# Performance work log

Hardware: AMD Instinct MI355X
Metric: run time of the kernel (lower is better)

## Reference

```python
import jax, jax.numpy as jnp
import numpy as np

N_A, N_P, N_T = 40000, 100000, 20000
D = 128
OUT = 64
E_AP, E_PT = 500000, 800000


def setup_inputs() -> dict:
    key = jax.random.key(0)
    ks = jax.random.split(key, 24)
    s = 1.0 / np.sqrt(D)
    inp = {
        'x_author': jax.random.normal(ks[0], (N_A, D), jnp.float32),
        'x_paper': jax.random.normal(ks[1], (N_P, D), jnp.float32),
        'x_term': jax.random.normal(ks[2], (N_T, D), jnp.float32),
        'W_l': jax.random.normal(ks[3], (3, 2, 4, D, D), jnp.float32) * s,
        'b_l': jax.random.normal(ks[4], (3, 2, 4, D), jnp.float32) * 0.01,
        'W_r': jax.random.normal(ks[5], (3, 2, 4, D, D), jnp.float32) * s,
        'lin_model_W': jax.random.normal(ks[6], (D, OUT), jnp.float32) * s,
        'lin_model_b': jax.random.normal(ks[7], (OUT,), jnp.float32) * 0.01,
        'lin_temp_W': jax.random.normal(ks[8], (D, OUT), jnp.float32) * s,
        'lin_temp_b': jax.random.normal(ks[9], (OUT,), jnp.float32) * 0.01,
        'lin2_W': jax.random.normal(ks[10], (OUT, 1), jnp.float32) * (1.0 / np.sqrt(OUT)),
        'lin2_b': jnp.ones((1,), jnp.float32),
        'src_ap': jax.random.randint(ks[11], (E_AP,), 0, N_A, jnp.int32),
        'dst_ap': jax.random.randint(ks[12], (E_AP,), 0, N_P, jnp.int32),
        'src_pa': jax.random.randint(ks[13], (E_AP,), 0, N_P, jnp.int32),
        'dst_pa': jax.random.randint(ks[14], (E_AP,), 0, N_A, jnp.int32),
        'src_pt': jax.random.randint(ks[15], (E_PT,), 0, N_P, jnp.int32),
        'dst_pt': jax.random.randint(ks[16], (E_PT,), 0, N_T, jnp.int32),
        'src_tp': jax.random.randint(ks[17], (E_PT,), 0, N_T, jnp.int32),
        'dst_tp': jax.random.randint(ks[18], (E_PT,), 0, N_P, jnp.int32),
    }
    return inp


def _sage(x_src, x_dst, src, dst, n_dst, Wl, bl, Wr):
    # PyG SAGEConv: lin_l(mean_aggr(x_j)) + lin_r(x_dst); lin_r has no bias.
    xj = x_src[src]                                         # [E, D] gather
    ssum = jax.ops.segment_sum(xj, dst, num_segments=n_dst)  # [n_dst, D]
    cnt = jax.ops.segment_sum(jnp.ones((src.shape[0],), x_src.dtype), dst,
                              num_segments=n_dst)
    mean = ssum / jnp.maximum(cnt, 1.0)[:, None]
    return mean @ Wl + bl + x_dst @ Wr


def _hetero_stack(xa, xp, xt, Wl, bl, Wr, edges, relu=True):
    # Wl/bl/Wr: [num_layers, 4, ...]; relation order: a->p, p->a, p->t, t->p.
    (sap, dap, spa, dpa, spt, dpt, stp, dtp) = edges
    n_layers = Wl.shape[0]
    for l in range(n_layers):
        p_new = (_sage(xa, xp, sap, dap, N_P, Wl[l, 0], bl[l, 0], Wr[l, 0])
                 + _sage(xt, xp, stp, dtp, N_P, Wl[l, 3], bl[l, 3], Wr[l, 3]))
        a_new = _sage(xp, xa, spa, dpa, N_A, Wl[l, 1], bl[l, 1], Wr[l, 1])
        t_new = _sage(xp, xt, spt, dpt, N_T, Wl[l, 2], bl[l, 2], Wr[l, 2])
        xa, xp, xt = jax.nn.relu(a_new), jax.nn.relu(p_new), jax.nn.relu(t_new)
    return xa, xp, xt


def reference(x_author, x_paper, x_term, W_l, b_l, W_r,
              lin_model_W, lin_model_b, lin_temp_W, lin_temp_b,
              lin2_W, lin2_b,
              src_ap, dst_ap, src_pa, dst_pa, src_pt, dst_pt, src_tp, dst_tp):
    edges = (src_ap, dst_ap, src_pa, dst_pa, src_pt, dst_pt, src_tp, dst_tp)
    # stack 0: self.model (DBLP) on raw features
    ma, mp, mt = _hetero_stack(x_author, x_paper, x_term,
                               W_l[0], b_l[0], W_r[0], edges)
    logits = ma @ lin_model_W + lin_model_b                  # [N_A, OUT]
    # stack 1: graph_temperature_scale (DBLP) on model's hidden x_dict
    ta, tp_, tt = _hetero_stack(ma, mp, mt, W_l[1], b_l[1], W_r[1], edges)
    ll1 = ta @ lin_temp_W + lin_temp_b                       # [N_A, OUT]
    temperature = ll1 @ lin2_W + lin2_b                      # [N_A, 1]
    # stack 2: self.convs on raw features (dropout = identity in eval mode)
    oa, op, ot = _hetero_stack(x_author, x_paper, x_term,
                               W_l[2], b_l[2], W_r[2], edges)
    return logits / temperature, oa, op, ot
```

## Files before the change

### kernel.cpp

```cpp
#include <hip/hip_runtime.h>
#include <cstdint>

#define N_A 40000
#define N_P 100000
#define N_T 20000
#define D 128
#define OUT_DIM 64
#define E_AP 500000
#define E_PT 800000

typedef __attribute__((ext_vector_type(8))) short bf16x8;
typedef __attribute__((ext_vector_type(4))) float f32x4;

static inline int ceil_div(int a, int b){ return (a + b - 1) / b; }

__device__ inline unsigned short f2bf(float f){
  uint32_t u = __builtin_bit_cast(uint32_t, f);
  uint32_t r = (u + 0x7FFFu + ((u >> 16) & 1u)) >> 16;
  return (unsigned short)r;
}
__device__ inline float bf2f(unsigned short h){
  uint32_t u = ((uint32_t)h) << 16;
  return __builtin_bit_cast(float, u);
}

__global__ void hist_kernel(const int* __restrict__ dst, int E, int* __restrict__ cnt){
  int i = blockIdx.x * blockDim.x + threadIdx.x;
  if (i < E) atomicAdd(&cnt[dst[i]], 1);
}

__global__ void block_sums_kernel(const int* __restrict__ cnt, int n, int* __restrict__ bsums){
  __shared__ int red[256];
  int b = blockIdx.x, t = threadIdx.x;
  int base = b * 1024;
  int s = 0;
  for (int i = t; i < 1024; i += 256){ int idx = base + i; if (idx < n) s += cnt[idx]; }
  red[t] = s; __syncthreads();
  for (int off = 128; off > 0; off >>= 1){ if (t < off) red[t] += red[t + off]; __syncthreads(); }
  if (t == 0) bsums[b] = red[0];
}

__global__ void scan_bsums_kernel(int* bsums, int nb){
  __shared__ int sh[128];
  int t = threadIdx.x;
  int v = (t < nb) ? bsums[t] : 0;
  sh[t] = v; __syncthreads();
  int inc = v;
  for (int off = 1; off < 128; off <<= 1){
    int x = (t >= off) ? sh[t - off] : 0; __syncthreads();
    inc += x; sh[t] = inc; __syncthreads();
  }
  if (t < nb) bsums[t] = inc - v;
}

__global__ void scan_final_kernel(const int* __restrict__ cnt, int n, const int* __restrict__ bsums,
                                  int* __restrict__ rowptr, int E){
  __shared__ int sh[256];
  int b = blockIdx.x, t = threadIdx.x;
  int base = b * 1024 + t * 4;
  int v[4]; int s = 0;
  #pragma unroll
  for (int j = 0; j < 4; j++){ int idx = base + j; v[j] = (idx < n) ? cnt[idx] : 0; s += v[j]; }
  sh[t] = s; __syncthreads();
  int inc = s;
  for (int off = 1; off < 256; off <<= 1){
    int x = (t >= off) ? sh[t - off] : 0; __syncthreads();
    inc += x; sh[t] = inc; __syncthreads();
  }
  int run = inc - s + bsums[b];
  #pragma unroll
  for (int j = 0; j < 4; j++){ int idx = base + j; if (idx < n) rowptr[idx] = run; run += v[j]; }
  if (b == 0 && t == 0) rowptr[n] = E;
}

__global__ void cursor_inv_kernel(const int* __restrict__ rowptr, const int* __restrict__ cnt,
                                  int n, int* __restrict__ cursor, float* __restrict__ inv){
  int i = blockIdx.x * blockDim.x + threadIdx.x;
  if (i < n){
    cursor[i] = rowptr[i];
    int c = cnt[i];
    inv[i] = 1.0f / (float)(c > 0 ? c : 1);
  }
}

__global__ void fill_kernel(const int* __restrict__ src, const int* __restrict__ dst, int E,
                            int* __restrict__ cursor, int* __restrict__ eidx){
  int i = blockIdx.x * blockDim.x + threadIdx.x;
  if (i < E){
    int d = dst[i];
    int pos = atomicAdd(&cursor[d], 1);
    eidx[pos] = src[i];
  }
}

__global__ void combine_wr_kernel(const float* __restrict__ Wr, float* __restrict__ wrc){
  int i = blockIdx.x * blockDim.x + threadIdx.x;
  if (i < 6 * D * D){
    int sl = i >> 14; int off = i & (D * D - 1);
    wrc[i] = Wr[(size_t)(sl * 4 + 0) * D * D + off] + Wr[(size_t)(sl * 4 + 3) * D * D + off];
  }
}

__global__ void combine_bias_kernel(const float* __restrict__ bl, float* __restrict__ bcomb){
  int i = blockIdx.x * blockDim.x + threadIdx.x;
  if (i < 6 * D){
    int sl = i >> 7; int off = i & (D - 1);
    bcomb[i] = bl[(size_t)(sl * 4 + 0) * D + off] + bl[(size_t)(sl * 4 + 3) * D + off];
  }
}

__global__ __launch_bounds__(256)
void pack_weights_kernel(const float* __restrict__ W_l, const float* __restrict__ W_r,
                         const float* __restrict__ wrc, const float* __restrict__ linW,
                         unsigned short* __restrict__ packs){
  int id = blockIdx.x;
  const float* src; int N = 128;
  if (id < 24)      src = W_l + (size_t)id * 16384;
  else if (id < 48) src = W_r + (size_t)(id - 24) * 16384;
  else if (id < 54) src = wrc + (size_t)(id - 48) * 16384;
  else            { src = linW; N = 64; }
  unsigned short* dhi = packs + (size_t)id * 32768;
  unsigned short* dlo = dhi + 16384;
  int ncf = N / 16;
  int slots = 4 * ncf * 64;
  for (int s = threadIdx.x; s < slots; s += 256){
    int frag = s >> 6, l = s & 63;
    int kc = frag / ncf, cf = frag - kc * ncf;
    int kb = kc * 32 + ((l >> 4) * 8);
    int col = cf * 16 + (l & 15);
    bf16x8 hv, lv;
    #pragma unroll
    for (int i = 0; i < 8; ++i){
      float f = src[(size_t)(kb + i) * N + col];
      unsigned short h = f2bf(f);
      hv[i] = (short)h;
      lv[i] = (short)f2bf(f - bf2f(h));
    }
    *(bf16x8*)(dhi + (size_t)s * 8) = hv;
    *(bf16x8*)(dlo + (size_t)s * 8) = lv;
  }
}

__global__ __launch_bounds__(256)
void agg_mean_kernel(const int* __restrict__ rowptr, const int* __restrict__ eidx,
                     const float* __restrict__ inv, const float* __restrict__ xsrc,
                     float* __restrict__ out, int ndst){
  int w = (blockIdx.x * blockDim.x + threadIdx.x) >> 6;
  if (w >= ndst) return;
  int l = threadIdx.x & 63;
  int p = l >> 5, kk = l & 31;
  int beg = rowptr[w], end = rowptr[w + 1];
  float4 a0 = make_float4(0,0,0,0), a1 = make_float4(0,0,0,0);
  float4 a2 = make_float4(0,0,0,0), a3 = make_float4(0,0,0,0);
  int e = beg;
  for (; e + 8 <= end; e += 8){
    int s0 = eidx[e + p], s1 = eidx[e + 2 + p], s2 = eidx[e + 4 + p], s3 = eidx[e + 6 + p];
    float4 v0 = ((const float4*)(xsrc + (size_t)s0 * D))[kk];
    float4 v1 = ((const float4*)(xsrc + (size_t)s1 * D))[kk];
    float4 v2 = ((const float4*)(xsrc + (size_t)s2 * D))[kk];
    float4 v3 = ((const float4*)(xsrc + (size_t)s3 * D))[kk];
    a0.x += v0.x; a0.y += v0.y; a0.z += v0.z; a0.w += v0.w;
    a1.x += v1.x; a1.y += v1.y; a1.z += v1.z; a1.w += v1.w;
    a2.x += v2.x; a2.y += v2.y; a2.z += v2.z; a2.w += v2.w;
    a3.x += v3.x; a3.y += v3.y; a3.z += v3.z; a3.w += v3.w;
  }
  if (e + 4 <= end){
    int s0 = eidx[e + p], s1 = eidx[e + 2 + p];
    float4 v0 = ((const float4*)(xsrc + (size_t)s0 * D))[kk];
    float4 v1 = ((const float4*)(xsrc + (size_t)s1 * D))[kk];
    a0.x += v0.x; a0.y += v0.y; a0.z += v0.z; a0.w += v0.w;
    a1.x += v1.x; a1.y += v1.y; a1.z += v1.z; a1.w += v1.w;
    e += 4;
  }
  if (e + 2 <= end){
    int s0 = eidx[e + p];
    float4 v0 = ((const float4*)(xsrc + (size_t)s0 * D))[kk];
    a0.x += v0.x; a0.y += v0.y; a0.z += v0.z; a0.w += v0.w;
    e += 2;
  }
  if (e < end && p == 0){
    int s0 = eidx[e];
    float4 v0 = ((const float4*)(xsrc + (size_t)s0 * D))[kk];
    a0.x += v0.x; a0.y += v0.y; a0.z += v0.z; a0.w += v0.w;
  }
  a0.x += a1.x + a2.x + a3.x; a0.y += a1.y + a2.y + a3.y;
  a0.z += a1.z + a2.z + a3.z; a0.w += a1.w + a2.w + a3.w;
  a0.x += __shfl_xor(a0.x, 32); a0.y += __shfl_xor(a0.y, 32);
  a0.z += __shfl_xor(a0.z, 32); a0.w += __shfl_xor(a0.w, 32);
  if (p == 0){
    float iv = inv[w];
    float4 r; r.x = a0.x * iv; r.y = a0.y * iv; r.z = a0.z * iv; r.w = a0.w * iv;
    ((float4*)(out + (size_t)w * D))[kk] = r;
  }
}

template<int NIN, int NCF, bool RELU, bool DIV>
__global__ __launch_bounds__(256)
void gemm_mfma(const float* __restrict__ in0, const unsigned short* hi0, const unsigned short* lo0,
               const float* __restrict__ in1, const unsigned short* hi1, const unsigned short* lo1,
               const float* __restrict__ in2, const unsigned short* hi2, const unsigned short* lo2,
               const float* __restrict__ bias, const float* __restrict__ tdiv,
               float* __restrict__ out, int nrows){
  const int tid  = threadIdx.x;
  const int w    = tid >> 6;
  const int l    = tid & 63;
  const int lane15 = l & 15;
  const int colg   = l >> 4;
  const int rbase  = blockIdx.x * 128 + w * 32;

  f32x4 acc[2][NCF];
  #pragma unroll
  for (int m = 0; m < 2; ++m)
    #pragma unroll
    for (int cf = 0; cf < NCF; ++cf) acc[m][cf] = (f32x4){0.f, 0.f, 0.f, 0.f};

  const float* ins[3]          = {in0, in1, in2};
  const unsigned short* his[3] = {hi0, hi1, hi2};
  const unsigned short* los[3] = {lo0, lo1, lo2};

  #pragma unroll
  for (int inp = 0; inp < NIN; ++inp){
    const float* A = ins[inp];
    const bf16x8* WH = (const bf16x8*)his[inp];
    const bf16x8* WL = (const bf16x8*)los[inp];
    #pragma unroll
    for (int kc = 0; kc < 4; ++kc){
      bf16x8 ah[2], al[2];
      #pragma unroll
      for (int m = 0; m < 2; ++m){
        int gr = rbase + m * 16 + lane15; if (gr >= nrows) gr = nrows - 1;
        const float4* p = (const float4*)(A + (size_t)gr * 128 + kc * 32 + colg * 8);
        float4 v0 = p[0], v1 = p[1];
        float fs[8] = {v0.x, v0.y, v0.z, v0.w, v1.x, v1.y, v1.z, v1.w};
        #pragma unroll
        for (int i = 0; i < 8; ++i){
          uint32_t u = __builtin_bit_cast(uint32_t, fs[i]);
          unsigned short h = (unsigned short)(u >> 16);
          float r = fs[i] - __builtin_bit_cast(float, u & 0xFFFF0000u);
          ah[m][i] = (short)h;
          al[m][i] = (short)(__builtin_bit_cast(uint32_t, r) >> 16);
        }
      }
      #pragma unroll
      for (int cf = 0; cf < NCF; ++cf){
        bf16x8 bh = WH[(kc * NCF + cf) * 64 + l];
        bf16x8 bl = WL[(kc * NCF + cf) * 64 + l];
        #pragma unroll
        for (int m = 0; m < 2; ++m){
          acc[m][cf] = __builtin_amdgcn_mfma_f32_16x16x32_bf16(ah[m], bh, acc[m][cf], 0, 0, 0);
          acc[m][cf] = __builtin_amdgcn_mfma_f32_16x16x32_bf16(al[m], bh, acc[m][cf], 0, 0, 0);
          acc[m][cf] = __builtin_amdgcn_mfma_f32_16x16x32_bf16(ah[m], bl, acc[m][cf], 0, 0, 0);
        }
      }
    }
  }

  #pragma unroll
  for (int cf = 0; cf < NCF; ++cf){
    int col = cf * 16 + lane15;
    float bv = bias[col];
    #pragma unroll
    for (int m = 0; m < 2; ++m){
      #pragma unroll
      for (int i = 0; i < 4; ++i){
        int gr = rbase + m * 16 + colg * 4 + i;
        if (gr < nrows){
          float v = acc[m][cf][i] + bv;
          if (RELU) v = fmaxf(v, 0.f);
          if (DIV)  v = v / tdiv[gr];
          out[(size_t)gr * (NCF * 16) + col] = v;
        }
      }
    }
  }
}

__global__ void wtc_kernel(const float* __restrict__ Wt, const float* __restrict__ bt,
                           const float* __restrict__ W2, const float* __restrict__ b2,
                           float* __restrict__ wtc){
  int k = threadIdx.x;
  if (k < 128){
    float s = 0.f;
    #pragma unroll 4
    for (int j = 0; j < 64; ++j) s += Wt[k * 64 + j] * W2[j];
    wtc[k] = s;
  }
  if (k == 0){
    float s = 0.f;
    for (int j = 0; j < 64; ++j) s += bt[j] * W2[j];
    wtc[128] = s + b2[0];
  }
}

__global__ __launch_bounds__(256)
void temp_kernel(const float* __restrict__ ta, const float* __restrict__ wtc,
                 float* __restrict__ temp, int n){
  int w = (blockIdx.x * blockDim.x + threadIdx.x) >> 6;
  if (w >= n) return;
  int l = threadIdx.x & 63;
  float2 v = ((const float2*)(ta + (size_t)w * D))[l];
  float2 c = ((const float2*)wtc)[l];
  float s = v.x * c.x + v.y * c.y;
  #pragma unroll
  for (int off = 32; off > 0; off >>= 1) s += __shfl_xor(s, off);
  if (l == 0) temp[w] = s + wtc[128];
}

extern "C" void kernel_launch(void* const* d_in, const int* in_sizes, int n_in,
                              void* d_out, int out_size, void* d_ws, size_t ws_size,
                              hipStream_t stream){
  const float* x_author    = (const float*)d_in[0];
  const float* x_paper     = (const float*)d_in[1];
  const float* x_term      = (const float*)d_in[2];
  const float* W_l         = (const float*)d_in[3];
  const float* b_l         = (const float*)d_in[4];
  const float* W_r         = (const float*)d_in[5];
  const float* lin_model_W = (const float*)d_in[6];
  const float* lin_model_b = (const float*)d_in[7];
  const float* lin_temp_W  = (const float*)d_in[8];
  const float* lin_temp_b  = (const float*)d_in[9];
  const float* lin2_W      = (const float*)d_in[10];
  const float* lin2_b      = (const float*)d_in[11];
  const int* src_ap = (const int*)d_in[12];
  const int* dst_ap = (const int*)d_in[13];
  const int* src_pa = (const int*)d_in[14];
  const int* dst_pa = (const int*)d_in[15];
  const int* src_pt = (const int*)d_in[16];
  const int* dst_pt = (const int*)d_in[17];
  const int* src_tp = (const int*)d_in[18];
  const int* dst_tp = (const int*)d_in[19];

  char* wp = (char*)d_ws;
  auto alloc = [&](size_t bytes)->void*{
    void* r = (void*)wp; wp += (bytes + 255) & ~(size_t)255; return r;
  };
  int*   rowptr_ap = (int*)alloc((N_P + 1) * 4);
  int*   cnt_ap    = (int*)alloc(N_P * 4);
  int*   cur_ap    = (int*)alloc(N_P * 4);
  int*   eidx_ap   = (int*)alloc((size_t)E_AP * 4);
  float* inv_ap    = (float*)alloc(N_P * 4);
  int*   rowptr_pa = (int*)alloc((N_A + 1) * 4);
  int*   cnt_pa    = (int*)alloc(N_A * 4);
  int*   cur_pa    = (int*)alloc(N_A * 4);
  int*   eidx_pa   = (int*)alloc((size_t)E_AP * 4);
  float* inv_pa    = (float*)alloc(N_A * 4);
  int*   rowptr_pt = (int*)alloc((N_T + 1) * 4);
  int*   cnt_pt    = (int*)alloc(N_T * 4);
  int*   cur_pt    = (int*)alloc(N_T * 4);
  int*   eidx_pt   = (int*)alloc((size_t)E_PT * 4);
  float* inv_pt    = (float*)alloc(N_T * 4);
  int*   rowptr_tp = (int*)alloc((N_P + 1) * 4);
  int*   cnt_tp    = (int*)alloc(N_P * 4);
  int*   cur_tp    = (int*)alloc(N_P * 4);
  int*   eidx_tp   = (int*)alloc((size_t)E_PT * 4);
  float* inv_tp    = (float*)alloc(N_P * 4);
  int*   bsums     = (int*)alloc(1024 * 4);
  float* A0    = (float*)alloc((size_t)N_A * D * 4);
  float* A1    = (float*)alloc((size_t)N_A * D * 4);
  float* TA    = (float*)alloc((size_t)N_A * D * 4);
  float* aggA  = (float*)alloc((size_t)N_A * D * 4);
  float* P0    = (float*)alloc((size_t)N_P * D * 4);
  float* P1    = (float*)alloc((size_t)N_P * D * 4);
  float* aggP1 = (float*)alloc((size_t)N_P * D * 4);
  float* aggP2 = (float*)alloc((size_t)N_P * D * 4);
  float* T0    = (float*)alloc((size_t)N_T * D * 4);
  float* T1    = (float*)alloc((size_t)N_T * D * 4);
  float* aggT  = (float*)alloc((size_t)N_T * D * 4);
  float* wrc   = (float*)alloc((size_t)6 * D * D * 4);
  float* bcomb = (float*)alloc((size_t)6 * D * 4);
  unsigned short* packs = (unsigned short*)alloc((size_t)55 * 32768 * 2);
  float* wtc   = (float*)alloc(129 * 4);
  float* temp  = (float*)alloc((size_t)N_A * 4);

  auto build = [&](const int* src, const int* dst, int E, int n,
                   int* rowptr, int* cnt, int* cursor, int* eidx, float* inv){
    hipMemsetAsync(cnt, 0, (size_t)n * 4, stream);
    hist_kernel<<<ceil_div(E, 256), 256, 0, stream>>>(dst, E, cnt);
    int nb = ceil_div(n, 1024);
    block_sums_kernel<<<nb, 256, 0, stream>>>(cnt, n, bsums);
    scan_bsums_kernel<<<1, 128, 0, stream>>>(bsums, nb);
    scan_final_kernel<<<nb, 256, 0, stream>>>(cnt, n, bsums, rowptr, E);
    cursor_inv_kernel<<<ceil_div(n, 256), 256, 0, stream>>>(rowptr, cnt, n, cursor, inv);
    fill_kernel<<<ceil_div(E, 256), 256, 0, stream>>>(src, dst, E, cursor, eidx);
  };
  build(src_ap, dst_ap, E_AP, N_P, rowptr_ap, cnt_ap, cur_ap, eidx_ap, inv_ap);
  build(src_pa, dst_pa, E_AP, N_A, rowptr_pa, cnt_pa, cur_pa, eidx_pa, inv_pa);
  build(src_pt, dst_pt, E_PT, N_T, rowptr_pt, cnt_pt, cur_pt, eidx_pt, inv_pt);
  build(src_tp, dst_tp, E_PT, N_P, rowptr_tp, cnt_tp, cur_tp, eidx_tp, inv_tp);

  combine_wr_kernel<<<ceil_div(6 * D * D, 256), 256, 0, stream>>>(W_r, wrc);
  combine_bias_kernel<<<ceil_div(6 * D, 256), 256, 0, stream>>>(b_l, bcomb);
  pack_weights_kernel<<<55, 256, 0, stream>>>(W_l, W_r, wrc, lin_model_W, packs);
  wtc_kernel<<<1, 128, 0, stream>>>(lin_temp_W, lin_temp_b, lin2_W, lin2_b, wtc);

  auto HI = [&](int id){ return packs + (size_t)id * 32768; };
  auto LO = [&](int id){ return packs + (size_t)id * 32768 + 16384; };
  auto IDL = [&](int s, int l, int r){ return (s * 2 + l) * 4 + r; };
  auto IDR = [&](int s, int l, int r){ return 24 + (s * 2 + l) * 4 + r; };
  auto IDC = [&](int s, int l){ return 48 + s * 2 + l; };
  auto Bl  = [&](int s, int l, int r){ return b_l + (size_t)((s * 2 + l) * 4 + r) * D; };
  auto BC  = [&](int s, int l){ return bcomb + (size_t)(s * 2 + l) * D; };

  auto agg = [&](const int* rowptr, const int* eidx, const float* inv,
                 const float* xsrc, float* outp, int ndst){
    agg_mean_kernel<<<ceil_div(ndst, 4), 256, 0, stream>>>(rowptr, eidx, inv, xsrc, outp, ndst);
  };

  auto layer = [&](const float* ia, const float* ip, const float* it, int s, int l,
                   float* oa, float* op, float* ot){
    if (op){
      agg(rowptr_ap, eidx_ap, inv_ap, ia, aggP1, N_P);
      agg(rowptr_tp, eidx_tp, inv_tp, it, aggP2, N_P);
      gemm_mfma<3, 8, true, false><<<ceil_div(N_P, 128), 256, 0, stream>>>(
          aggP1, HI(IDL(s, l, 0)), LO(IDL(s, l, 0)),
          aggP2, HI(IDL(s, l, 3)), LO(IDL(s, l, 3)),
          ip,    HI(IDC(s, l)),    LO(IDC(s, l)),
          BC(s, l), nullptr, op, N_P);
    }
    if (oa){
      agg(rowptr_pa, eidx_pa, inv_pa, ip, aggA, N_A);
      gemm_mfma<2, 8, true, false><<<ceil_div(N_A, 128), 256, 0, stream>>>(
          aggA, HI(IDL(s, l, 1)), LO(IDL(s, l, 1)),
          ia,   HI(IDR(s, l, 1)), LO(IDR(s, l, 1)),
          nullptr, nullptr, nullptr,
          Bl(s, l, 1), nullptr, oa, N_A);
    }
    if (ot){
      agg(rowptr_pt, eidx_pt, inv_pt, ip, aggT, N_T);
      gemm_mfma<2, 8, true, false><<<ceil_div(N_T, 128), 256, 0, stream>>>(
          aggT, HI(IDL(s, l, 2)), LO(IDL(s, l, 2)),
          it,   HI(IDR(s, l, 2)), LO(IDR(s, l, 2)),
          nullptr, nullptr, nullptr,
          Bl(s, l, 2), nullptr, ot, N_T);
    }
  };

  float* out_logits = (float*)d_out;
  float* out_oa = out_logits + (size_t)N_A * OUT_DIM;
  float* out_op = out_oa + (size_t)N_A * D;
  float* out_ot = out_op + (size_t)N_P * D;

  layer(x_author, x_paper, x_term, 0, 0, A1, P1, T1);
  layer(A1, P1, T1, 0, 1, A0, P0, T0);
  layer(A0, P0, T0, 1, 0, A1, P1, T1);
  layer(A1, P1, T1, 1, 1, TA, nullptr, nullptr);
  layer(x_author, x_paper, x_term, 2, 0, A1, P1, T1);
  layer(A1, P1, T1, 2, 1, out_oa, out_op, out_ot);
  temp_kernel<<<ceil_div(N_A, 4), 256, 0, stream>>>(TA, wtc, temp, N_A);
  gemm_mfma<1, 4, false, true><<<ceil_div(N_A, 128), 256, 0, stream>>>(
      A0, HI(54), LO(54),
      nullptr, nullptr, nullptr,
      nullptr, nullptr, nullptr,
      lin_model_b, temp, out_logits, N_A);
}
```

Before: 2.452 ms.

## Share raw-feature aggregation across stacks and retile MFMA GEMM to 64x64 waves

```diff
diff --git a/kernel.cpp b/kernel.cpp
--- a/kernel.cpp
+++ b/kernel.cpp
@@ -194,25 +194,28 @@
   }
 }
 
-template<int NIN, int NCF, bool RELU, bool DIV>
+template<int NIN, int NCFT, bool RELU, bool DIV>
 __global__ __launch_bounds__(256)
 void gemm_mfma(const float* __restrict__ in0, const unsigned short* hi0, const unsigned short* lo0,
                const float* __restrict__ in1, const unsigned short* hi1, const unsigned short* lo1,
                const float* __restrict__ in2, const unsigned short* hi2, const unsigned short* lo2,
                const float* __restrict__ bias, const float* __restrict__ tdiv,
                float* __restrict__ out, int nrows){
-  const int tid  = threadIdx.x;
-  const int w    = tid >> 6;
-  const int l    = tid & 63;
+  constexpr int WC = NCFT / 4;
+  constexpr int WR = 4 / WC;
+  const int tid    = threadIdx.x;
+  const int w      = tid >> 6;
+  const int l      = tid & 63;
   const int lane15 = l & 15;
   const int colg   = l >> 4;
-  const int rbase  = blockIdx.x * 128 + w * 32;
-
-  f32x4 acc[2][NCF];
-  #pragma unroll
-  for (int m = 0; m < 2; ++m)
+  const int wr     = w / WC, wc = w % WC;
+  const int rbase  = blockIdx.x * (WR * 64) + wr * 64;
+
+  f32x4 acc[4][4];
+  #pragma unroll
+  for (int m = 0; m < 4; ++m)
     #pragma unroll
-    for (int cf = 0; cf < NCF; ++cf) acc[m][cf] = (f32x4){0.f, 0.f, 0.f, 0.f};
+    for (int cf = 0; cf < 4; ++cf) acc[m][cf] = (f32x4){0.f, 0.f, 0.f, 0.f};
 
   const float* ins[3]          = {in0, in1, in2};
   const unsigned short* his[3] = {hi0, hi1, hi2};
@@ -225,9 +228,16 @@
     const bf16x8* WL = (const bf16x8*)los[inp];
     #pragma unroll
     for (int kc = 0; kc < 4; ++kc){
-      bf16x8 ah[2], al[2];
+      bf16x8 bh[4], bl[4];
       #pragma unroll
-      for (int m = 0; m < 2; ++m){
+      for (int cf = 0; cf < 4; ++cf){
+        int idx = (kc * NCFT + wc * 4 + cf) * 64 + l;
+        bh[cf] = WH[idx];
+        bl[cf] = WL[idx];
+      }
+      bf16x8 ah[4], al[4];
+      #pragma unroll
+      for (int m = 0; m < 4; ++m){
         int gr = rbase + m * 16 + lane15; if (gr >= nrows) gr = nrows - 1;
         const float4* p = (const float4*)(A + (size_t)gr * 128 + kc * 32 + colg * 8);
         float4 v0 = p[0], v1 = p[1];
@@ -242,25 +252,23 @@
         }
       }
       #pragma unroll
-      for (int cf = 0; cf < NCF; ++cf){
-        bf16x8 bh = WH[(kc * NCF + cf) * 64 + l];
-        bf16x8 bl = WL[(kc * NCF + cf) * 64 + l];
+      for (int cf = 0; cf < 4; ++cf){
         #pragma unroll
-        for (int m = 0; m < 2; ++m){
-          acc[m][cf] = __builtin_amdgcn_mfma_f32_16x16x32_bf16(ah[m], bh, acc[m][cf], 0, 0, 0);
-          acc[m][cf] = __builtin_amdgcn_mfma_f32_16x16x32_bf16(al[m], bh, acc[m][cf], 0, 0, 0);
-          acc[m][cf] = __builtin_amdgcn_mfma_f32_16x16x32_bf16(ah[m], bl, acc[m][cf], 0, 0, 0);
+        for (int m = 0; m < 4; ++m){
+          acc[m][cf] = __builtin_amdgcn_mfma_f32_16x16x32_bf16(ah[m], bh[cf], acc[m][cf], 0, 0, 0);
+          acc[m][cf] = __builtin_amdgcn_mfma_f32_16x16x32_bf16(al[m], bh[cf], acc[m][cf], 0, 0, 0);
+          acc[m][cf] = __builtin_amdgcn_mfma_f32_16x16x32_bf16(ah[m], bl[cf], acc[m][cf], 0, 0, 0);
         }
       }
     }
   }
 
   #pragma unroll
-  for (int cf = 0; cf < NCF; ++cf){
-    int col = cf * 16 + lane15;
+  for (int cf = 0; cf < 4; ++cf){
+    int col = (wc * 4 + cf) * 16 + lane15;
     float bv = bias[col];
     #pragma unroll
-    for (int m = 0; m < 2; ++m){
+    for (int m = 0; m < 4; ++m){
       #pragma unroll
       for (int i = 0; i < 4; ++i){
         int gr = rbase + m * 16 + colg * 4 + i;
@@ -268,7 +276,7 @@
           float v = acc[m][cf][i] + bv;
           if (RELU) v = fmaxf(v, 0.f);
           if (DIV)  v = v / tdiv[gr];
-          out[(size_t)gr * (NCF * 16) + col] = v;
+          out[(size_t)gr * (NCFT * 16) + col] = v;
         }
       }
     }
@@ -355,22 +363,25 @@
   int*   eidx_tp   = (int*)alloc((size_t)E_PT * 4);
   float* inv_tp    = (float*)alloc(N_P * 4);
   int*   bsums     = (int*)alloc(1024 * 4);
-  float* A0    = (float*)alloc((size_t)N_A * D * 4);
-  float* A1    = (float*)alloc((size_t)N_A * D * 4);
-  float* TA    = (float*)alloc((size_t)N_A * D * 4);
-  float* aggA  = (float*)alloc((size_t)N_A * D * 4);
-  float* P0    = (float*)alloc((size_t)N_P * D * 4);
-  float* P1    = (float*)alloc((size_t)N_P * D * 4);
-  float* aggP1 = (float*)alloc((size_t)N_P * D * 4);
-  float* aggP2 = (float*)alloc((size_t)N_P * D * 4);
-  float* T0    = (float*)alloc((size_t)N_T * D * 4);
-  float* T1    = (float*)alloc((size_t)N_T * D * 4);
-  float* aggT  = (float*)alloc((size_t)N_T * D * 4);
+  unsigned short* packs = (unsigned short*)alloc((size_t)55 * 32768 * 2);
   float* wrc   = (float*)alloc((size_t)6 * D * D * 4);
   float* bcomb = (float*)alloc((size_t)6 * D * 4);
-  unsigned short* packs = (unsigned short*)alloc((size_t)55 * 32768 * 2);
   float* wtc   = (float*)alloc(129 * 4);
   float* temp  = (float*)alloc((size_t)N_A * 4);
+  float* gA  = (float*)alloc((size_t)N_A * D * 4);
+  float* gP1 = (float*)alloc((size_t)N_P * D * 4);
+  float* gP2 = (float*)alloc((size_t)N_P * D * 4);
+  float* gT  = (float*)alloc((size_t)N_T * D * 4);
+  float* A1 = (float*)alloc((size_t)N_A * D * 4);
+  float* P1 = (float*)alloc((size_t)N_P * D * 4);
+  float* T1 = (float*)alloc((size_t)N_T * D * 4);
+  float* A2 = (float*)alloc((size_t)N_A * D * 4);
+  float* P2 = (float*)alloc((size_t)N_P * D * 4);
+  float* T2 = (float*)alloc((size_t)N_T * D * 4);
+  float* A0 = A2;
+  float* P0 = P2;
+  float* T0 = T2;
+  float* TA = P2;
 
   auto build = [&](const int* src, const int* dst, int E, int n,
                    int* rowptr, int* cnt, int* cursor, int* eidx, float* inv){
@@ -406,33 +417,30 @@
     agg_mean_kernel<<<ceil_div(ndst, 4), 256, 0, stream>>>(rowptr, eidx, inv, xsrc, outp, ndst);
   };
 
-  auto layer = [&](const float* ia, const float* ip, const float* it, int s, int l,
+  auto agg_all = [&](const float* ia, const float* ip, const float* it){
+    agg(rowptr_ap, eidx_ap, inv_ap, ia, gP1, N_P);
+    agg(rowptr_tp, eidx_tp, inv_tp, it, gP2, N_P);
+    agg(rowptr_pa, eidx_pa, inv_pa, ip, gA, N_A);
+    agg(rowptr_pt, eidx_pt, inv_pt, ip, gT, N_T);
+  };
+
+  auto gemms = [&](const float* ia, const float* ip, const float* it, int s, int l,
                    float* oa, float* op, float* ot){
-    if (op){
-      agg(rowptr_ap, eidx_ap, inv_ap, ia, aggP1, N_P);
-      agg(rowptr_tp, eidx_tp, inv_tp, it, aggP2, N_P);
-      gemm_mfma<3, 8, true, false><<<ceil_div(N_P, 128), 256, 0, stream>>>(
-          aggP1, HI(IDL(s, l, 0)), LO(IDL(s, l, 0)),
-          aggP2, HI(IDL(s, l, 3)), LO(IDL(s, l, 3)),
-          ip,    HI(IDC(s, l)),    LO(IDC(s, l)),
-          BC(s, l), nullptr, op, N_P);
-    }
-    if (oa){
-      agg(rowptr_pa, eidx_pa, inv_pa, ip, aggA, N_A);
-      gemm_mfma<2, 8, true, false><<<ceil_div(N_A, 128), 256, 0, stream>>>(
-          aggA, HI(IDL(s, l, 1)), LO(IDL(s, l, 1)),
-          ia,   HI(IDR(s, l, 1)), LO(IDR(s, l, 1)),
-          nullptr, nullptr, nullptr,
-          Bl(s, l, 1), nullptr, oa, N_A);
-    }
-    if (ot){
-      agg(rowptr_pt, eidx_pt, inv_pt, ip, aggT, N_T);
-      gemm_mfma<2, 8, true, false><<<ceil_div(N_T, 128), 256, 0, stream>>>(
-          aggT, HI(IDL(s, l, 2)), LO(IDL(s, l, 2)),
-          it,   HI(IDR(s, l, 2)), LO(IDR(s, l, 2)),
-          nullptr, nullptr, nullptr,
-          Bl(s, l, 2), nullptr, ot, N_T);
-    }
+    if (op) gemm_mfma<3, 8, true, false><<<ceil_div(N_P, 128), 256, 0, stream>>>(
+        gP1, HI(IDL(s, l, 0)), LO(IDL(s, l, 0)),
+        gP2, HI(IDL(s, l, 3)), LO(IDL(s, l, 3)),
+        ip,  HI(IDC(s, l)),    LO(IDC(s, l)),
+        BC(s, l), nullptr, op, N_P);
+    if (oa) gemm_mfma<2, 8, true, false><<<ceil_div(N_A, 128), 256, 0, stream>>>(
+        gA, HI(IDL(s, l, 1)), LO(IDL(s, l, 1)),
+        ia, HI(IDR(s, l, 1)), LO(IDR(s, l, 1)),
+        nullptr, nullptr, nullptr,
+        Bl(s, l, 1), nullptr, oa, N_A);
+    if (ot) gemm_mfma<2, 8, true, false><<<ceil_div(N_T, 128), 256, 0, stream>>>(
+        gT, HI(IDL(s, l, 2)), LO(IDL(s, l, 2)),
+        it, HI(IDR(s, l, 2)), LO(IDR(s, l, 2)),
+        nullptr, nullptr, nullptr,
+        Bl(s, l, 2), nullptr, ot, N_T);
   };
 
   float* out_logits = (float*)d_out;
@@ -440,14 +448,23 @@
   float* out_op = out_oa + (size_t)N_A * D;
   float* out_ot = out_op + (size_t)N_P * D;
 
-  layer(x_author, x_paper, x_term, 0, 0, A1, P1, T1);
-  layer(A1, P1, T1, 0, 1, A0, P0, T0);
-  layer(A0, P0, T0, 1, 0, A1, P1, T1);
-  layer(A1, P1, T1, 1, 1, TA, nullptr, nullptr);
-  layer(x_author, x_paper, x_term, 2, 0, A1, P1, T1);
-  layer(A1, P1, T1, 2, 1, out_oa, out_op, out_ot);
+  agg_all(x_author, x_paper, x_term);
+  gemms(x_author, x_paper, x_term, 0, 0, A1, P1, T1);
+  gemms(x_author, x_paper, x_term, 2, 0, A2, P2, T2);
+  agg_all(A2, P2, T2);
+  gemms(A2, P2, T2, 2, 1, out_oa, out_op, out_ot);
+  agg_all(A1, P1, T1);
+  gemms(A1, P1, T1, 0, 1, A0, P0, T0);
+  agg_all(A0, P0, T0);
+  gemms(A0, P0, T0, 1, 0, A1, P1, T1);
+  agg(rowptr_pa, eidx_pa, inv_pa, P1, gA, N_A);
+  gemm_mfma<2, 8, true, false><<<ceil_div(N_A, 128), 256, 0, stream>>>(
+      gA, HI(IDL(1, 1, 1)), LO(IDL(1, 1, 1)),
+      A1, HI(IDR(1, 1, 1)), LO(IDR(1, 1, 1)),
+      nullptr, nullptr, nullptr,
+      Bl(1, 1, 1), nullptr, TA, N_A);
   temp_kernel<<<ceil_div(N_A, 4), 256, 0, stream>>>(TA, wtc, temp, N_A);
-  gemm_mfma<1, 4, false, true><<<ceil_div(N_A, 128), 256, 0, stream>>>(
+  gemm_mfma<1, 4, false, true><<<ceil_div(N_A, 256), 256, 0, stream>>>(
       A0, HI(54), LO(54),
       nullptr, nullptr, nullptr,
       nullptr, nullptr, nullptr,
```

After: 2.158 ms. -12.0%, faster.
